# Optimization experiments

Measured on AMD Instinct MI355X. Metric: run time of the kernel, lower is better.

The kernel has to match this reference:

```python
import jax, jax.numpy as jnp
import numpy as np

D_MODEL = 768
N_HEADS = 12
D_K = D_MODEL // N_HEADS


def setup_inputs() -> dict:
    key = jax.random.key(0)
    kq, kk, kv, kwq, kbq, kwo, kbo = jax.random.split(key, 7)
    B, S = 1, 4096
    s = 1.0 / np.sqrt(D_MODEL)
    return {
        "q": jax.random.normal(kq, (B, S, D_MODEL), jnp.float32),
        "k": jax.random.normal(kk, (B, S, D_MODEL), jnp.float32),
        "v": jax.random.normal(kv, (B, S, D_MODEL), jnp.float32),
        # nn.Linear weights stored as [out, in]; note the original forward
        # uses W_q for Q, K, AND V (W_k/W_v are never used), so only W_q and
        # W_o are materialized here.
        "Wq": jax.random.uniform(kwq, (D_MODEL, D_MODEL), jnp.float32, -s, s),
        "bq": jax.random.uniform(kbq, (D_MODEL,), jnp.float32, -s, s),
        "Wo": jax.random.uniform(kwo, (D_MODEL, D_MODEL), jnp.float32, -s, s),
        "bo": jax.random.uniform(kbo, (D_MODEL,), jnp.float32, -s, s),
    }


def _split_heads(x):  # [B,S,D] -> [B,H,S,Dk]
    B, S, _ = x.shape
    return x.reshape(B, S, N_HEADS, D_K).transpose(0, 2, 1, 3)


def reference(q, k, v, Wq, bq, Wo, bo):
    # Faithful to source: same W_q projection applied to q, k, v.
    Q = _split_heads(q @ Wq.T + bq)
    K = _split_heads(k @ Wq.T + bq)
    V = _split_heads(v @ Wq.T + bq)
    scale = 1.0 / np.sqrt(D_K).astype(np.float32)
    scores = jnp.einsum("bhqd,bhkd->bhqk", Q, K) * scale  # [B,H,S,S]
    probs = jax.nn.softmax(scores, axis=-1)
    atten = jnp.einsum("bhqk,bhkd->bhqd", probs, V)
    B, _, S, _ = atten.shape
    concat = atten.transpose(0, 2, 1, 3).reshape(B, S, D_MODEL)
    return concat @ Wo.T + bo
```

## Files before the change

### kernel.cpp

```cpp
#include <hip/hip_runtime.h>
#include <stdint.h>
#include <math.h>


#define SQ 4096
#define DM 768
#define NH 12

typedef float f32x4 __attribute__((ext_vector_type(4)));
typedef short bf16x8 __attribute__((ext_vector_type(8)));
typedef unsigned int u32x4 __attribute__((ext_vector_type(4)));
typedef unsigned short ushort_t;

static __device__ __forceinline__ ushort_t f2bf(float f) {
    unsigned int u = __builtin_bit_cast(unsigned int, f);
    u += 0x7fffu + ((u >> 16) & 1u);
    return (ushort_t)(u >> 16);
}

static __device__ __forceinline__ unsigned int cvt_pk_bf16(float a, float b) {
    unsigned int d;
    asm("v_cvt_pk_bf16_f32 %0, %1, %2" : "=v"(d) : "v"(a), "v"(b));
    return d;
}

static __device__ __forceinline__ float exp2_hw(float x) {
    float r;
    asm("v_exp_f32 %0, %1" : "=v"(r) : "v"(x));
    return r;
}

static __device__ __forceinline__ void gload16(const ushort_t* g, ushort_t* l) {
    __builtin_amdgcn_global_load_lds(
        reinterpret_cast<const __attribute__((address_space(1))) unsigned int*>(
            reinterpret_cast<uintptr_t>(g)),
        reinterpret_cast<__attribute__((address_space(3))) unsigned int*>(
            reinterpret_cast<uintptr_t>(l)),
        16, 0, 0);
}

__global__ __launch_bounds__(256) void cvt_all(
    const float* __restrict__ q, const float* __restrict__ k,
    const float* __restrict__ v, const float* __restrict__ Wq,
    const float* __restrict__ Wo, ushort_t* __restrict__ xb,
    ushort_t* __restrict__ wqb, ushort_t* __restrict__ wob) {
    const int NE4 = (SQ * DM) / 4;
    const int NW4 = (DM * DM) / 4;
    int i = blockIdx.x * 256 + threadIdx.x;
    const float* src;
    ushort_t* dst;
    if (i < NE4) { src = q; dst = xb; }
    else if (i < 2 * NE4) { src = k; dst = xb + SQ * DM; i -= NE4; }
    else if (i < 3 * NE4) { src = v; dst = xb + 2 * SQ * DM; i -= 2 * NE4; }
    else if (i < 3 * NE4 + NW4) { src = Wq; dst = wqb; i -= 3 * NE4; }
    else if (i < 3 * NE4 + 2 * NW4) { src = Wo; dst = wob; i -= 3 * NE4 + NW4; }
    else return;
    float4 x = reinterpret_cast<const float4*>(src)[i];
    ushort4 o;
    o.x = f2bf(x.x); o.y = f2bf(x.y); o.z = f2bf(x.z); o.w = f2bf(x.w);
    reinterpret_cast<ushort4*>(dst)[i] = o;
}

template <int EPI>
__global__ __launch_bounds__(256) void gemm_bf16(
    const ushort_t* __restrict__ A, const ushort_t* __restrict__ B,
    const float* __restrict__ bias, ushort_t* __restrict__ proj,
    ushort_t* __restrict__ vt, float* __restrict__ outf) {
    __shared__ __align__(16) ushort_t lsA[128 * 64];
    __shared__ __align__(16) ushort_t lsB[128 * 64];
    const int tid = threadIdx.x;
    const int lane = tid & 63;
    const int w = tid >> 6;
    const int wm = w >> 1, wn = w & 1;
    const int g = lane >> 4, li = lane & 15;
    const int bm = blockIdx.x / 6, bn = blockIdx.x % 6;
    const int arow = bm * 128, brow = bn * 128;
    const int sr = lane >> 3;
    const int sc = ((lane & 7) ^ sr) * 8;

    f32x4 acc[4][4] = {};

    for (int kt = 0; kt < 12; ++kt) {
        const int k0 = kt * 64;
        __syncthreads();
#pragma unroll
        for (int c = 0; c < 4; ++c) {
            const int chunk = w * 4 + c;
            const int r = chunk * 8 + sr;
            gload16(A + (size_t)(arow + r) * DM + k0 + sc, lsA + chunk * 512);
            gload16(B + (size_t)(brow + r) * DM + k0 + sc, lsB + chunk * 512);
        }
        __syncthreads();

        bf16x8 af[4][2];
#pragma unroll
        for (int mf = 0; mf < 4; ++mf) {
            const int row = wm * 64 + mf * 16 + li;
#pragma unroll
            for (int ks = 0; ks < 2; ++ks)
                af[mf][ks] = *reinterpret_cast<const bf16x8*>(
                    lsA + row * 64 + ((ks * 32 + g * 8) ^ ((li & 7) << 3)));
        }
#pragma unroll
        for (int nf = 0; nf < 4; ++nf) {
            const int row = wn * 64 + nf * 16 + li;
            bf16x8 b0 = *reinterpret_cast<const bf16x8*>(
                lsB + row * 64 + ((g * 8) ^ ((li & 7) << 3)));
            bf16x8 b1 = *reinterpret_cast<const bf16x8*>(
                lsB + row * 64 + ((32 + g * 8) ^ ((li & 7) << 3)));
#pragma unroll
            for (int mf = 0; mf < 4; ++mf) {
                acc[mf][nf] = __builtin_amdgcn_mfma_f32_16x16x32_bf16(af[mf][0], b0, acc[mf][nf], 0, 0, 0);
                acc[mf][nf] = __builtin_amdgcn_mfma_f32_16x16x32_bf16(af[mf][1], b1, acc[mf][nf], 0, 0, 0);
            }
        }
    }

    if (EPI == 0) {
        const bool isV = (arow >= 8192);
        const float qscale = (arow < 4096) ? 0.18033688011112042f : 1.0f;
#pragma unroll
        for (int nf = 0; nf < 4; ++nf) {
            const int col = brow + wn * 64 + nf * 16 + li;
            const float bv = bias[col];
#pragma unroll
            for (int mf = 0; mf < 4; ++mf) {
                const int row0 = arow + wm * 64 + mf * 16 + g * 4;
                if (!isV) {
#pragma unroll
                    for (int r = 0; r < 4; ++r)
                        proj[(size_t)(row0 + r) * DM + col] = f2bf((acc[mf][nf][r] + bv) * qscale);
                } else {
                    ushort4 pk;
                    pk.x = f2bf(acc[mf][nf][0] + bv);
                    pk.y = f2bf(acc[mf][nf][1] + bv);
                    pk.z = f2bf(acc[mf][nf][2] + bv);
                    pk.w = f2bf(acc[mf][nf][3] + bv);
                    const int kv = row0 - 8192;
                    const int pos = (kv & ~31) | ((kv & 0xC) << 1) | (((kv >> 4) & 1) << 2);
                    *reinterpret_cast<ushort4*>(vt + (size_t)col * SQ + pos) = pk;
                }
            }
        }
    } else {
#pragma unroll
        for (int nf = 0; nf < 4; ++nf) {
            const int col = brow + wn * 64 + nf * 16 + li;
            const float bv = bias[col];
#pragma unroll
            for (int mf = 0; mf < 4; ++mf) {
                const int row0 = arow + wm * 64 + mf * 16 + g * 4;
#pragma unroll
                for (int r = 0; r < 4; ++r)
                    outf[(size_t)(row0 + r) * DM + col] = acc[mf][nf][r] + bv;
            }
        }
    }
}

__global__ __launch_bounds__(256) void attn_bf16(
    const ushort_t* __restrict__ qk, const ushort_t* __restrict__ vtb,
    ushort_t* __restrict__ cc) {
    __shared__ __align__(16) ushort_t kl[2][2][32 * 64];
    __shared__ __align__(16) ushort_t vl[2][2][64 * 32];

    const int tid = threadIdx.x, lane = tid & 63, w = tid >> 6;
    const int wp = w & 1, p = w >> 1;
    const int g = lane >> 4, li = lane & 15;
    const int logical = (blockIdx.x & 7) * 96 + (blockIdx.x >> 3);
    const int h = logical >> 6, qb = logical & 63;
    const int sr = lane >> 3;
    const int sc = ((lane & 7) ^ sr) * 8;
    const int vdr = lane >> 2;
    const int vsc = ((lane & 3) ^ (vdr & 3)) * 8;

    const ushort_t* Kb = qk + (size_t)(4096 + p * 2048) * DM + (size_t)h * 64;
    const ushort_t* Vb = vtb + (size_t)(h * 64) * SQ + p * 2048;

    bf16x8 qf[2][2];
#pragma unroll
    for (int qh = 0; qh < 2; ++qh)
#pragma unroll
        for (int ks = 0; ks < 2; ++ks)
            qf[qh][ks] = *reinterpret_cast<const bf16x8*>(
                qk + (size_t)(qb * 64 + wp * 32 + qh * 16 + li) * DM + h * 64 + ks * 32 + g * 8);

    f32x4 oacc[2][4] = {};
    float lsum0 = 0.f, lsum1 = 0.f;

#pragma unroll
    for (int c = 0; c < 2; ++c) {
        const int ch = wp * 2 + c;
        gload16(Kb + (size_t)(ch * 8 + sr) * DM + sc, &kl[p][0][ch * 512]);
        gload16(Vb + (size_t)(ch * 16 + vdr) * SQ + vsc, &vl[p][0][ch * 512]);
    }
    __syncthreads();

#define STEP(kp, vp, kn, vn, kvn)                                              \
    do {                                                                       \
        if ((kvn) < 64) {                                                      \
            const int kvo = (kvn) * 32;                                        \
            _Pragma("unroll") for (int c = 0; c < 2; ++c) {                    \
                const int ch = wp * 2 + c;                                     \
                gload16(Kb + (size_t)(kvo + ch * 8 + sr) * DM + sc,            \
                        &(kn)[ch * 512]);                                      \
                gload16(Vb + (size_t)(ch * 16 + vdr) * SQ + kvo + vsc,         \
                        &(vn)[ch * 512]);                                      \
            }                                                                  \
        }                                                                      \
        f32x4 sf[2][2] = {};                                                   \
        __builtin_amdgcn_s_setprio(1);                                         \
        _Pragma("unroll") for (int nf = 0; nf < 2; ++nf) {                     \
            const int row = nf * 16 + li;                                      \
            bf16x8 kb0 = *reinterpret_cast<const bf16x8*>(                     \
                (kp) + row * 64 + ((g * 8) ^ ((li & 7) << 3)));                \
            bf16x8 kb1 = *reinterpret_cast<const bf16x8*>(                     \
                (kp) + row * 64 + ((32 + g * 8) ^ ((li & 7) << 3)));           \
            _Pragma("unroll") for (int qh = 0; qh < 2; ++qh) {                 \
                sf[qh][nf] = __builtin_amdgcn_mfma_f32_16x16x32_bf16(          \
                    kb0, qf[qh][0], sf[qh][nf], 0, 0, 0);                      \
                sf[qh][nf] = __builtin_amdgcn_mfma_f32_16x16x32_bf16(          \
                    kb1, qf[qh][1], sf[qh][nf], 0, 0, 0);                      \
            }                                                                  \
        }                                                                      \
        __builtin_amdgcn_s_setprio(0);                                         \
        _Pragma("unroll") for (int qh = 0; qh < 2; ++qh)                       \
            _Pragma("unroll") for (int nf = 0; nf < 2; ++nf) {                 \
                f32x4 pe;                                                      \
                _Pragma("unroll") for (int r = 0; r < 4; ++r)                  \
                    pe[r] = exp2_hw(sf[qh][nf][r]);                            \
                sf[qh][nf] = pe;                                               \
                const float ps = (pe[0] + pe[1]) + (pe[2] + pe[3]);            \
                if (qh == 0) lsum0 += ps; else lsum1 += ps;                    \
            }                                                                  \
        __builtin_amdgcn_s_setprio(1);                                         \
        bf16x8 pa[2];                                                          \
        _Pragma("unroll") for (int qh = 0; qh < 2; ++qh) {                     \
            u32x4 pu;                                                          \
            pu.x = cvt_pk_bf16(sf[qh][0][0], sf[qh][0][1]);                    \
            pu.y = cvt_pk_bf16(sf[qh][0][2], sf[qh][0][3]);                    \
            pu.z = cvt_pk_bf16(sf[qh][1][0], sf[qh][1][1]);                    \
            pu.w = cvt_pk_bf16(sf[qh][1][2], sf[qh][1][3]);                    \
            pa[qh] = __builtin_bit_cast(bf16x8, pu);                           \
        }                                                                      \
        _Pragma("unroll") for (int nv = 0; nv < 4; ++nv) {                     \
            const int vrow = nv * 16 + li;                                     \
            bf16x8 vb = *reinterpret_cast<const bf16x8*>(                      \
                (vp) + vrow * 32 + ((g ^ (li & 3)) * 8));                      \
            oacc[0][nv] = __builtin_amdgcn_mfma_f32_16x16x32_bf16(             \
                pa[0], vb, oacc[0][nv], 0, 0, 0);                              \
            oacc[1][nv] = __builtin_amdgcn_mfma_f32_16x16x32_bf16(             \
                pa[1], vb, oacc[1][nv], 0, 0, 0);                              \
        }                                                                      \
        __builtin_amdgcn_s_setprio(0);                                         \
        __syncthreads();                                                       \
    } while (0)

    {
        ushort_t* k0p = &kl[p][0][0];
        ushort_t* v0p = &vl[p][0][0];
        ushort_t* k1p = &kl[p][1][0];
        ushort_t* v1p = &vl[p][1][0];
#pragma unroll 1
        for (int t = 0; t < 32; ++t) {
            STEP(k0p, v0p, k1p, v1p, 2 * t + 1);
            STEP(k1p, v1p, k0p, v0p, 2 * t + 2);
        }
    }
#undef STEP

    float* ob = reinterpret_cast<float*>(&kl[0][0][0]);
    float* lsb = ob + 4096;
    if (p == 1) {
#pragma unroll
        for (int qh = 0; qh < 2; ++qh) {
#pragma unroll
            for (int nv = 0; nv < 4; ++nv)
                *reinterpret_cast<f32x4*>(
                    ob + (((wp * 2 + qh) * 4 + nv) * 64 + lane) * 4) = oacc[qh][nv];
            lsb[(wp * 2 + qh) * 64 + lane] = (qh == 0) ? lsum0 : lsum1;
        }
    }
    __syncthreads();
    if (p == 0) {
        lsum0 += lsb[(wp * 2 + 0) * 64 + lane];
        lsum1 += lsb[(wp * 2 + 1) * 64 + lane];
#pragma unroll
        for (int qh = 0; qh < 2; ++qh)
#pragma unroll
            for (int nv = 0; nv < 4; ++nv) {
                f32x4 o = *reinterpret_cast<const f32x4*>(
                    ob + (((wp * 2 + qh) * 4 + nv) * 64 + lane) * 4);
                oacc[qh][nv] += o;
            }

#pragma unroll
        for (int qh = 0; qh < 2; ++qh) {
            float s = (qh == 0) ? lsum0 : lsum1;
            s += __shfl_xor(s, 16);
            s += __shfl_xor(s, 32);
            float inv[4];
            const int gbase = g << 2;
#pragma unroll
            for (int r = 0; r < 4; ++r)
                inv[r] = 1.0f / __shfl(s, gbase + r);
#pragma unroll
            for (int nv = 0; nv < 4; ++nv)
#pragma unroll
                for (int r = 0; r < 4; ++r) {
                    const int row = qb * 64 + wp * 32 + qh * 16 + g * 4 + r;
                    const int col = h * 64 + nv * 16 + li;
                    cc[(size_t)row * DM + col] = f2bf(oacc[qh][nv][r] * inv[r]);
                }
        }
    }
}

extern "C" void kernel_launch(void* const* d_in, const int* in_sizes, int n_in,
                              void* d_out, int out_size, void* d_ws, size_t ws_size,
                              hipStream_t stream) {
    const float* q = (const float*)d_in[0];
    const float* k = (const float*)d_in[1];
    const float* v = (const float*)d_in[2];
    const float* Wq = (const float*)d_in[3];
    const float* bq = (const float*)d_in[4];
    const float* Wo = (const float*)d_in[5];
    const float* bo = (const float*)d_in[6];
    float* out = (float*)d_out;

    ushort_t* ws = (ushort_t*)d_ws;
    const int NE = SQ * DM;
    ushort_t* xb = ws;
    ushort_t* wqb = ws + 3 * NE;
    ushort_t* wob = wqb + DM * DM;
    ushort_t* proj = wob + DM * DM;
    ushort_t* vt = proj + 2 * NE;
    ushort_t* cc = vt + NE;

    const int n4 = 3 * (NE / 4) + 2 * ((DM * DM) / 4);
    cvt_all<<<(n4 + 255) / 256, 256, 0, stream>>>(q, k, v, Wq, Wo, xb, wqb, wob);

    gemm_bf16<0><<<(12288 / 128) * 6, 256, 0, stream>>>(xb, wqb, bq, proj, vt, (float*)nullptr);

    attn_bf16<<<NH * (SQ / 64), 256, 0, stream>>>(proj, vt, cc);

    gemm_bf16<1><<<(SQ / 128) * 6, 256, 0, stream>>>(cc, wob, bo, (ushort_t*)nullptr, (ushort_t*)nullptr, out);
}
```

Measured before the change: 137.4 us.

## Compute V projection as transposed GEMM to write V^T with coalesced stores

The V projection is split out of the fused QKV GEMM into its own launch that computes W·V^T directly, with the weights as the A operand and the V activations as B. Bias is applied per row, and the output goes into the permuted V^T layout one element at a time along the sequence dimension. The aim is to replace the scattered 8-byte transposed stores in the old epilogue with contiguous writes along rows of V^T. The attention kernel's LDS swizzle for V is adjusted to match the new permutation. This adds one extra kernel launch and scalar 2-byte stores.

```diff
diff --git a/kernel.cpp b/kernel.cpp
--- a/kernel.cpp
+++ b/kernel.cpp
@@ -73,7 +73,8 @@
     const int w = tid >> 6;
     const int wm = w >> 1, wn = w & 1;
     const int g = lane >> 4, li = lane & 15;
-    const int bm = blockIdx.x / 6, bn = blockIdx.x % 6;
+    const int NB = (EPI == 2) ? 32 : 6;
+    const int bm = blockIdx.x / NB, bn = blockIdx.x % NB;
     const int arow = bm * 128, brow = bn * 128;
     const int sr = lane >> 3;
     const int sc = ((lane & 7) ^ sr) * 8;
@@ -117,7 +118,6 @@
     }
 
     if (EPI == 0) {
-        const bool isV = (arow >= 8192);
         const float qscale = (arow < 4096) ? 0.18033688011112042f : 1.0f;
 #pragma unroll
         for (int nf = 0; nf < 4; ++nf) {
@@ -126,20 +126,28 @@
 #pragma unroll
             for (int mf = 0; mf < 4; ++mf) {
                 const int row0 = arow + wm * 64 + mf * 16 + g * 4;
-                if (!isV) {
-#pragma unroll
-                    for (int r = 0; r < 4; ++r)
-                        proj[(size_t)(row0 + r) * DM + col] = f2bf((acc[mf][nf][r] + bv) * qscale);
-                } else {
-                    ushort4 pk;
-                    pk.x = f2bf(acc[mf][nf][0] + bv);
-                    pk.y = f2bf(acc[mf][nf][1] + bv);
-                    pk.z = f2bf(acc[mf][nf][2] + bv);
-                    pk.w = f2bf(acc[mf][nf][3] + bv);
-                    const int kv = row0 - 8192;
-                    const int pos = (kv & ~31) | ((kv & 0xC) << 1) | (((kv >> 4) & 1) << 2);
-                    *reinterpret_cast<ushort4*>(vt + (size_t)col * SQ + pos) = pk;
-                }
+#pragma unroll
+                for (int r = 0; r < 4; ++r)
+                    proj[(size_t)(row0 + r) * DM + col] = f2bf((acc[mf][nf][r] + bv) * qscale);
+            }
+        }
+    } else if (EPI == 2) {
+        float bv[4][4];
+#pragma unroll
+        for (int mf = 0; mf < 4; ++mf)
+#pragma unroll
+            for (int r = 0; r < 4; ++r)
+                bv[mf][r] = bias[arow + wm * 64 + mf * 16 + g * 4 + r];
+#pragma unroll
+        for (int nf = 0; nf < 4; ++nf) {
+            const int j = brow + wn * 64 + nf * 16 + li;
+            const int pos = (j & ~31) | ((j & 0xC) << 1) | (((j >> 4) & 1) << 2) | (j & 3);
+#pragma unroll
+            for (int mf = 0; mf < 4; ++mf) {
+                const int row0 = arow + wm * 64 + mf * 16 + g * 4;
+#pragma unroll
+                for (int r = 0; r < 4; ++r)
+                    vt[(size_t)(row0 + r) * SQ + pos] = f2bf(acc[mf][nf][r] + bv[mf][r]);
             }
         }
     } else {
@@ -172,7 +180,7 @@
     const int sr = lane >> 3;
     const int sc = ((lane & 7) ^ sr) * 8;
     const int vdr = lane >> 2;
-    const int vsc = ((lane & 3) ^ (vdr & 3)) * 8;
+    const int vsc = ((lane & 3) ^ ((lane >> 3) & 3)) * 8;
 
     const ushort_t* Kb = qk + (size_t)(4096 + p * 2048) * DM + (size_t)h * 64;
     const ushort_t* Vb = vtb + (size_t)(h * 64) * SQ + p * 2048;
@@ -246,7 +254,7 @@
         _Pragma("unroll") for (int nv = 0; nv < 4; ++nv) {                     \
             const int vrow = nv * 16 + li;                                     \
             bf16x8 vb = *reinterpret_cast<const bf16x8*>(                      \
-                (vp) + vrow * 32 + ((g ^ (li & 3)) * 8));                      \
+                (vp) + vrow * 32 + ((g ^ ((li >> 1) & 3)) * 8));               \
             oacc[0][nv] = __builtin_amdgcn_mfma_f32_16x16x32_bf16(             \
                 pa[0], vb, oacc[0][nv], 0, 0, 0);                              \
             oacc[1][nv] = __builtin_amdgcn_mfma_f32_16x16x32_bf16(             \
@@ -340,7 +348,9 @@
     const int n4 = 3 * (NE / 4) + 2 * ((DM * DM) / 4);
     cvt_all<<<(n4 + 255) / 256, 256, 0, stream>>>(q, k, v, Wq, Wo, xb, wqb, wob);
 
-    gemm_bf16<0><<<(12288 / 128) * 6, 256, 0, stream>>>(xb, wqb, bq, proj, vt, (float*)nullptr);
+    gemm_bf16<0><<<(8192 / 128) * 6, 256, 0, stream>>>(xb, wqb, bq, proj, (ushort_t*)nullptr, (float*)nullptr);
+
+    gemm_bf16<2><<<(768 / 128) * 32, 256, 0, stream>>>(wqb, xb + 2 * NE, bq, (ushort_t*)nullptr, vt, (float*)nullptr);
 
     attn_bf16<<<NH * (SQ / 64), 256, 0, stream>>>(proj, vt, cc);
 
```

After: 137.5 us. No clear change (+0.0%).
